# Performance work log

Hardware: AMD Instinct MI355X
Metric: run time of the kernel (lower is better)

The kernel has to match this reference:

```python
import jax, jax.numpy as jnp
import numpy as np
from jax import lax

_DN = ('NCHW', 'OIHW', 'NCHW')
_EPS = 1e-5


def _conv3x3(x, w):
    return lax.conv_general_dilated(x, w, (1, 1), ((1, 1), (1, 1)), dimension_numbers=_DN)


def _bn(x, gamma, beta):
    # BatchNorm2d in (torch-default) training mode: batch statistics over (B,H,W)
    mean = x.mean(axis=(0, 2, 3), keepdims=True)
    var = x.var(axis=(0, 2, 3), keepdims=True)
    return (x - mean) * lax.rsqrt(var + _EPS) * gamma[None, :, None, None] + beta[None, :, None, None]


def _g1(x, w1, g1g, g1b, w2, g2g, g2b):
    x = jax.nn.relu(_bn(_conv3x3(x, w1), g1g, g1b))
    return jax.nn.relu(_bn(_conv3x3(x, w2), g2g, g2b))


def _weight_volume(left2, right2, maxdisp):
    # left2/right2: [B,1,H,W]. For each column j, min over window
    # [max(0, j-maxdisp), min(W, j+maxdisp)) of |right - left[:, :, :, j]|.
    L = left2[:, 0]  # [B,H,W]
    R = right2[:, 0]
    W = L.shape[-1]
    d = jnp.arange(-maxdisp, maxdisp)              # exclusive right bound -> offsets [-D, D-1]
    idx = jnp.arange(W)[:, None] + d[None, :]       # [W, 2D]
    valid = (idx >= 0) & (idx < W)
    g = R[:, :, jnp.clip(idx, 0, W - 1)]            # [B,H,W,2D]
    diff = jnp.where(valid, jnp.abs(g - L[..., None]), jnp.inf)
    v = diff.min(axis=-1)                           # [B,H,W]
    return (1.0 - jax.nn.sigmoid(v))[:, None]       # [B,1,H,W]


def setup_inputs() -> dict:
    key = jax.random.key(0)
    ks = jax.random.split(key, 5)
    B, C, H, W = 4, 32, 256, 512
    return {
        'left': jax.random.normal(ks[0], (B, C, H, W), jnp.float32),
        'right': jax.random.normal(ks[1], (B, C, H, W), jnp.float32),
        'w1': jax.random.normal(ks[2], (C, C, 3, 3), jnp.float32) * 0.05,
        'bn1_g': jnp.ones((C,), jnp.float32),
        'bn1_b': jnp.zeros((C,), jnp.float32),
        'w2': jax.random.normal(ks[3], (C, C, 3, 3), jnp.float32) * 0.05,
        'bn2_g': jnp.ones((C,), jnp.float32),
        'bn2_b': jnp.zeros((C,), jnp.float32),
        'g2_w': jax.random.normal(ks[4], (1, C, 1, 1), jnp.float32) * 0.1,
        'g2_b': jnp.zeros((1,), jnp.float32),
        'maxdisp': 48,
    }


def reference(left, right, w1, bn1_g, bn1_b, w2, bn2_g, bn2_b, g2_w, g2_b, maxdisp):
    left_g1 = _g1(left, w1, bn1_g, bn1_b, w2, bn2_g, bn2_b)
    right_g1 = _g1(right, w1, bn1_g, bn1_b, w2, bn2_g, bn2_b)
    # g2: 1x1 conv with bias -> single channel
    left_g2 = lax.conv_general_dilated(left_g1, g2_w, (1, 1), ((0, 0), (0, 0)), dimension_numbers=_DN) + g2_b[None, :, None, None]
    right_g2 = lax.conv_general_dilated(right_g1, g2_w, (1, 1), ((0, 0), (0, 0)), dimension_numbers=_DN) + g2_b[None, :, None, None]
    left_weight = _weight_volume(left_g2, right_g2, maxdisp)
    right_weight = _weight_volume(right_g2, left_g2, maxdisp)
    left_out = left_g1 * left_weight + left
    right_out = right_g1 * right_weight + right
    return (left_out, right_out)
```

## Files before the change

### kernel.cpp

```cpp
#include <hip/hip_runtime.h>

#define CC 32
#define HH 256
#define WW 512
#define HWSZ (HH*WW)
#define BB 4
#define NIMG 8
#define EPS 1e-5f
#define MAXD 48

typedef __attribute__((ext_vector_type(8))) short short8;
typedef __attribute__((ext_vector_type(16))) float f32x16;

#define ACT_R 10
#define ACT_C 66
#define ACT_BLKS (4*ACT_R*ACT_C)
#define WL_BLKS (9*2*2*32)
#define ACT_BYTES (ACT_BLKS*16)
#define WL_BYTES (WL_BLKS*16)
#define SM_BYTES (ACT_BYTES + WL_BYTES)

__device__ inline unsigned short f2bf(float f) {
  unsigned int b = __builtin_bit_cast(unsigned int, f);
  b += 0x7FFFu + ((b >> 16) & 1u);
  return (unsigned short)(b >> 16);
}

template<bool FUSE>
__global__ __launch_bounds__(256, 2) void conv3x3_mfma_k(
    const float* __restrict__ inL, const float* __restrict__ inR,
    const float* __restrict__ yin, const float* __restrict__ wgt,
    const float* __restrict__ scale, const float* __restrict__ shift,
    float* __restrict__ yout, float* __restrict__ ssum, float* __restrict__ ssq)
{
  __shared__ __align__(16) char sm[SM_BYTES];
  short8* actb = (short8*)sm;
  short8* wlb  = (short8*)(sm + ACT_BYTES);

  const int tid = threadIdx.x;
  const int bx  = blockIdx.x;
  const int img = bx >> 8;
  const int rem = bx & 255;
  const int ty  = rem >> 3;
  const int tx  = rem & 7;
  const int y0  = ty * 8;
  const int x0  = tx * 64;
  const int side = img >> 2;

  const float* src = FUSE ? (yin + (size_t)img * CC * HWSZ)
                          : ((img < BB) ? inL + (size_t)img * CC * HWSZ
                                        : inR + (size_t)(img - BB) * CC * HWSZ);

  for (int e = tid; e < ACT_BLKS; e += 256) {
    int c  = e % ACT_C;
    int rg = e / ACT_C;
    int r  = rg % ACT_R;
    int g  = rg / ACT_R;
    int xx = x0 - 1 + c;
    int yy = y0 - 1 + r;
    short8 v;
    #pragma unroll
    for (int j = 0; j < 8; ++j) v[j] = 0;
    if ((unsigned)xx < (unsigned)WW && (unsigned)yy < (unsigned)HH) {
      const float* p = src + (size_t)(g * 8) * HWSZ + (size_t)yy * WW + xx;
      #pragma unroll
      for (int j = 0; j < 8; ++j) {
        float f = p[(size_t)j * HWSZ];
        if (FUSE) {
          f = fmaf(f, scale[side * CC + g * 8 + j], shift[side * CC + g * 8 + j]);
          f = fmaxf(f, 0.f);
        }
        v[j] = (short)f2bf(f);
      }
    }
    actb[e] = v;
  }
  for (int e = tid; e < WL_BLKS; e += 256) {
    int co = e & 31;
    int gg = e >> 5;
    int g2 = gg & 1;
    int st = gg >> 1;
    int t  = st & 1;
    int s  = st >> 1;
    int cib = t * 16 + g2 * 8;
    short8 v;
    #pragma unroll
    for (int j = 0; j < 8; ++j)
      v[j] = (short)f2bf(wgt[(size_t)(co * CC + cib + j) * 9 + s]);
    wlb[e] = v;
  }
  __syncthreads();

  const int l   = tid & 63;
  const int wid = tid >> 6;
  const int wr  = wid >> 1;
  const int wc  = wid & 1;
  const int lh  = l >> 5;
  const int ln  = l & 31;

  short8 afr[18];
  #pragma unroll
  for (int st = 0; st < 18; ++st)
    afr[st] = wlb[(st * 2 + lh) * 32 + ln];

  f32x16 acc[4];
  #pragma unroll
  for (int o = 0; o < 4; ++o)
    #pragma unroll
    for (int i = 0; i < 16; ++i) acc[o][i] = 0.f;

  const int cbase = wc * 32 + ln;
  #pragma unroll
  for (int irow = 0; irow < 6; ++irow) {
    const int rr = wr * 4 + irow;
    #pragma unroll
    for (int t = 0; t < 2; ++t) {
      #pragma unroll
      for (int kx = 0; kx < 3; ++kx) {
        short8 b = actb[((t * 2 + lh) * ACT_R + rr) * ACT_C + cbase + kx];
        #pragma unroll
        for (int ky = 0; ky < 3; ++ky) {
          const int o = irow - ky;
          if (o >= 0 && o <= 3) {
            acc[o] = __builtin_amdgcn_mfma_f32_32x32x16_bf16(
                       afr[(ky * 3 + kx) * 2 + t], b, acc[o], 0, 0, 0);
          }
        }
      }
    }
  }

  const int ox = x0 + wc * 32 + ln;
  const size_t ibase = (size_t)img * CC * HWSZ;
  #pragma unroll
  for (int o = 0; o < 4; ++o) {
    const int oy = y0 + wr * 4 + o;
    const size_t pb = ibase + (size_t)oy * WW + ox;
    #pragma unroll
    for (int r16 = 0; r16 < 16; ++r16) {
      const int co = (r16 & 3) + 8 * (r16 >> 2) + 4 * lh;
      yout[pb + (size_t)co * HWSZ] = acc[o][r16];
    }
  }

  float s16[16], q16[16];
  #pragma unroll
  for (int r16 = 0; r16 < 16; ++r16) {
    float s = 0.f, q = 0.f;
    #pragma unroll
    for (int o = 0; o < 4; ++o) { float v = acc[o][r16]; s += v; q += v * v; }
    #pragma unroll
    for (int off = 16; off >= 1; off >>= 1) {
      s += __shfl_xor(s, off);
      q += __shfl_xor(q, off);
    }
    s16[r16] = s; q16[r16] = q;
  }
  __syncthreads();
  float* sred = (float*)(sm + ACT_BYTES);
  if (ln == 0) {
    #pragma unroll
    for (int r16 = 0; r16 < 16; ++r16) {
      const int co = (r16 & 3) + 8 * (r16 >> 2) + 4 * lh;
      sred[wid * 64 + co]      = s16[r16];
      sred[wid * 64 + 32 + co] = q16[r16];
    }
  }
  __syncthreads();
  if (tid < 64) {
    float v = sred[tid] + sred[64 + tid] + sred[128 + tid] + sred[192 + tid];
    if (tid < 32) atomicAdd(&ssum[side * CC + tid], v);
    else          atomicAdd(&ssq [side * CC + tid - 32], v);
  }
}

__global__ __launch_bounds__(64) void bnfin_k(
    const float* __restrict__ ssum, const float* __restrict__ ssq,
    const float* __restrict__ gamma, const float* __restrict__ beta,
    float* __restrict__ scale, float* __restrict__ shift)
{
    int t = threadIdx.x;
    int c = t & 31;
    const float n = (float)(BB * HWSZ);
    float m  = ssum[t] / n;
    float vr = ssq[t] / n - m * m;
    float sc = gamma[c] * rsqrtf(vr + EPS);
    scale[t] = sc;
    shift[t] = beta[c] - m * sc;
}

__global__ __launch_bounds__(256) void g2_k(
    const float* __restrict__ y2, const float* __restrict__ scale, const float* __restrict__ shift,
    const float* __restrict__ g2w, const float* __restrict__ g2b, float* __restrict__ g2)
{
    size_t p4 = ((size_t)blockIdx.x * 256 + threadIdx.x) * 4;
    int img  = (int)(p4 >> 17);
    int side = img >> 2;
    size_t pp = p4 & (HWSZ - 1);
    float b0 = g2b[0];
    float4 accv = make_float4(b0, b0, b0, b0);
    #pragma unroll
    for (int c = 0; c < CC; ++c) {
        float4 v = *(const float4*)&y2[((size_t)img * CC + c) * HWSZ + pp];
        float s = scale[side * CC + c];
        float b = shift[side * CC + c];
        float w = g2w[c];
        accv.x += fmaxf(v.x * s + b, 0.f) * w;
        accv.y += fmaxf(v.y * s + b, 0.f) * w;
        accv.z += fmaxf(v.z * s + b, 0.f) * w;
        accv.w += fmaxf(v.w * s + b, 0.f) * w;
    }
    *(float4*)&g2[p4] = accv;
}

__global__ __launch_bounds__(256) void final_k(
    const float* __restrict__ y2, const float* __restrict__ scale, const float* __restrict__ shift,
    const float* __restrict__ g2, const float* __restrict__ left, const float* __restrict__ right,
    float* __restrict__ out)
{
    __shared__ float Lr[WW];
    __shared__ float Rr[WW];
    const int b = blockIdx.x >> 8;
    const int h = blockIdx.x & 255;
    const int tid = threadIdx.x;

    const size_t rowoff = (size_t)h * WW;
    Lr[tid]       = g2[(size_t)b * HWSZ + rowoff + tid];
    Lr[tid + 256] = g2[(size_t)b * HWSZ + rowoff + tid + 256];
    Rr[tid]       = g2[(size_t)(BB + b) * HWSZ + rowoff + tid];
    Rr[tid + 256] = g2[(size_t)(BB + b) * HWSZ + rowoff + tid + 256];
    __syncthreads();

    const size_t OUT_R = (size_t)BB * CC * HWSZ;

    for (int w = tid; w < WW; w += 256) {
        float Lv = Lr[w], Rv = Rr[w];
        float vL = 1e30f, vR = 1e30f;
        int lo = (w - MAXD < 0) ? 0 : (w - MAXD);
        int hi = (w + MAXD - 1 > WW - 1) ? (WW - 1) : (w + MAXD - 1);
        for (int idx = lo; idx <= hi; ++idx) {
            vL = fminf(vL, fabsf(Rr[idx] - Lv));
            vR = fminf(vR, fabsf(Lr[idx] - Rv));
        }
        float wL = 1.f / (1.f + __expf(vL));
        float wR = 1.f / (1.f + __expf(vR));

        const size_t pix = rowoff + w;
        #pragma unroll 4
        for (int c = 0; c < CC; ++c) {
            size_t ioff = ((size_t)b * CC + c) * HWSZ + pix;
            float zL = fmaxf(y2[((size_t)b * CC + c) * HWSZ + pix]        * scale[c]      + shift[c],      0.f);
            float zR = fmaxf(y2[((size_t)(BB + b) * CC + c) * HWSZ + pix] * scale[CC + c] + shift[CC + c], 0.f);
            out[ioff]         = zL * wL + left[ioff];
            out[OUT_R + ioff] = zR * wR + right[ioff];
        }
    }
}

extern "C" void kernel_launch(void* const* d_in, const int* in_sizes, int n_in,
                              void* d_out, int out_size, void* d_ws, size_t ws_size,
                              hipStream_t stream)
{
    const float* left  = (const float*)d_in[0];
    const float* right = (const float*)d_in[1];
    const float* w1    = (const float*)d_in[2];
    const float* bn1g  = (const float*)d_in[3];
    const float* bn1b  = (const float*)d_in[4];
    const float* w2    = (const float*)d_in[5];
    const float* bn2g  = (const float*)d_in[6];
    const float* bn2b  = (const float*)d_in[7];
    const float* g2w   = (const float*)d_in[8];
    const float* g2b   = (const float*)d_in[9];
    float* out = (float*)d_out;
    float* ws  = (float*)d_ws;

    const size_t YSZ = (size_t)NIMG * CC * HWSZ;
    float* y1    = ws;
    float* y2    = ws + YSZ;
    float* stats = ws + 2 * YSZ;
    float* g2buf = ws;

    float* sum1 = stats;       float* sq1 = stats + 64;
    float* sum2 = stats + 128; float* sq2 = stats + 192;
    float* sc1  = stats + 256; float* sh1 = stats + 320;
    float* sc2  = stats + 384; float* sh2 = stats + 448;

    hipMemsetAsync(stats, 0, 512 * sizeof(float), stream);

    conv3x3_mfma_k<false><<<2048, 256, 0, stream>>>(left, right, nullptr, w1,
                                                    nullptr, nullptr, y1, sum1, sq1);
    bnfin_k<<<1, 64, 0, stream>>>(sum1, sq1, bn1g, bn1b, sc1, sh1);
    conv3x3_mfma_k<true><<<2048, 256, 0, stream>>>(nullptr, nullptr, y1, w2,
                                                   sc1, sh1, y2, sum2, sq2);
    bnfin_k<<<1, 64, 0, stream>>>(sum2, sq2, bn2g, bn2b, sc2, sh2);
    g2_k<<<1024, 256, 0, stream>>>(y2, sc2, sh2, g2w, g2b, g2buf);
    final_k<<<1024, 256, 0, stream>>>(y2, sc2, sh2, g2buf, left, right, out);
}
```

Measured before the change: 512.5 us.

## Store activations as channel-packed bf16 NHWC and fuse g2 into final kernel

Adds a pre-pass that converts inputs to bf16 channel-interleaved (8 channels per 16-byte vector) layout and pre-packs weights once, so the conv kernels load contiguous short8 vectors instead of eight strided fp32 loads. Intermediate conv outputs are stored as packed bf16, halving intermediate traffic. The g2 1x1 conv is fused into the final kernel via shared memory, removing a full read of y2 and a separate launch. It adds an extra transpose pass and stores y1/y2 in bf16, which lowers intermediate precision.

```diff
diff --git a/kernel.cpp b/kernel.cpp
--- a/kernel.cpp
+++ b/kernel.cpp
@@ -9,99 +9,121 @@
 #define EPS 1e-5f
 #define MAXD 48
 
-typedef __attribute__((ext_vector_type(8))) short short8;
-typedef __attribute__((ext_vector_type(16))) float f32x16;
-
 #define ACT_R 10
 #define ACT_C 66
-#define ACT_BLKS (4*ACT_R*ACT_C)
-#define WL_BLKS (9*2*2*32)
-#define ACT_BYTES (ACT_BLKS*16)
-#define WL_BYTES (WL_BLKS*16)
-#define SM_BYTES (ACT_BYTES + WL_BYTES)
+
+typedef __attribute__((ext_vector_type(8))) short short8;
+typedef __attribute__((ext_vector_type(4))) short short4v;
+typedef __attribute__((ext_vector_type(16))) float f32x16;
 
 __device__ inline unsigned short f2bf(float f) {
   unsigned int b = __builtin_bit_cast(unsigned int, f);
   b += 0x7FFFu + ((b >> 16) & 1u);
   return (unsigned short)(b >> 16);
 }
-
-template<bool FUSE>
-__global__ __launch_bounds__(256, 2) void conv3x3_mfma_k(
+__device__ inline float bf2f(short s) {
+  unsigned int u = ((unsigned int)(unsigned short)s) << 16;
+  return __builtin_bit_cast(float, u);
+}
+
+__global__ __launch_bounds__(256) void wxpose_k(
+    const float* __restrict__ w1, const float* __restrict__ w2,
+    short8* __restrict__ wtr)
+{
+  int e = blockIdx.x * 256 + threadIdx.x;
+  if (e >= 2304) return;
+  int which = e >= 1152;
+  int i = e - which * 1152;
+  const float* w = which ? w2 : w1;
+  int ln = i & 31, lh = (i >> 5) & 1, t = (i >> 6) & 1, s = i >> 7;
+  short8 v;
+  #pragma unroll
+  for (int j = 0; j < 8; ++j)
+    v[j] = (short)f2bf(w[(size_t)(ln * CC + t * 16 + lh * 8 + j) * 9 + s]);
+  wtr[e] = v;
+}
+
+__global__ __launch_bounds__(256) void xpose_k(
     const float* __restrict__ inL, const float* __restrict__ inR,
-    const float* __restrict__ yin, const float* __restrict__ wgt,
+    short8* __restrict__ xin)
+{
+  const int img = blockIdx.x >> 8;
+  const int y   = blockIdx.x & 255;
+  const int g   = threadIdx.x >> 6;
+  const int xl  = threadIdx.x & 63;
+  const float* src = (img < BB ? inL : inR) + (size_t)(img & 3) * CC * HWSZ + (size_t)y * WW;
+  short8* dst = xin + ((size_t)img * HH + y) * WW * 4;
+  #pragma unroll
+  for (int xc = 0; xc < 8; ++xc) {
+    int x = xc * 64 + xl;
+    short8 v;
+    #pragma unroll
+    for (int j = 0; j < 8; ++j)
+      v[j] = (short)f2bf(src[(size_t)(g * 8 + j) * HWSZ + x]);
+    dst[(size_t)x * 4 + g] = v;
+  }
+}
+
+template<bool NORM>
+__global__ __launch_bounds__(256, 3) void conv_k(
+    const short8* __restrict__ xin, const short8* __restrict__ wtab,
     const float* __restrict__ scale, const float* __restrict__ shift,
-    float* __restrict__ yout, float* __restrict__ ssum, float* __restrict__ ssq)
-{
-  __shared__ __align__(16) char sm[SM_BYTES];
-  short8* actb = (short8*)sm;
-  short8* wlb  = (short8*)(sm + ACT_BYTES);
-
-  const int tid = threadIdx.x;
-  const int bx  = blockIdx.x;
-  const int img = bx >> 8;
-  const int rem = bx & 255;
-  const int ty  = rem >> 3;
-  const int tx  = rem & 7;
-  const int y0  = ty * 8;
-  const int x0  = tx * 64;
+    short8* __restrict__ yout, float* __restrict__ ssum, float* __restrict__ ssq)
+{
+  __shared__ short8 actb[4 * ACT_R * ACT_C];
+  __shared__ float sred[256];
+
+  const int tid  = threadIdx.x;
+  const int img  = blockIdx.x >> 8;
+  const int rem  = blockIdx.x & 255;
+  const int y0   = (rem >> 3) * 8;
+  const int x0   = (rem & 7) * 64;
   const int side = img >> 2;
-
-  const float* src = FUSE ? (yin + (size_t)img * CC * HWSZ)
-                          : ((img < BB) ? inL + (size_t)img * CC * HWSZ
-                                        : inR + (size_t)(img - BB) * CC * HWSZ);
-
-  for (int e = tid; e < ACT_BLKS; e += 256) {
-    int c  = e % ACT_C;
-    int rg = e / ACT_C;
-    int r  = rg % ACT_R;
-    int g  = rg / ACT_R;
-    int xx = x0 - 1 + c;
-    int yy = y0 - 1 + r;
-    short8 v;
-    #pragma unroll
-    for (int j = 0; j < 8; ++j) v[j] = 0;
-    if ((unsigned)xx < (unsigned)WW && (unsigned)yy < (unsigned)HH) {
-      const float* p = src + (size_t)(g * 8) * HWSZ + (size_t)yy * WW + xx;
-      #pragma unroll
-      for (int j = 0; j < 8; ++j) {
-        float f = p[(size_t)j * HWSZ];
-        if (FUSE) {
-          f = fmaf(f, scale[side * CC + g * 8 + j], shift[side * CC + g * 8 + j]);
-          f = fmaxf(f, 0.f);
+  const int wid  = tid >> 6;
+  const int lane = tid & 63;
+
+  float scg[8], shg[8];
+  if (NORM) {
+    #pragma unroll
+    for (int j = 0; j < 8; ++j) {
+      scg[j] = scale[side * CC + wid * 8 + j];
+      shg[j] = shift[side * CC + wid * 8 + j];
+    }
+  }
+
+  const short8* srcimg = xin + (size_t)img * HH * WW * 4;
+  #pragma unroll
+  for (int i = 0; i < 11; ++i) {
+    int e = lane + i * 64;
+    if (e < ACT_R * ACT_C) {
+      int r  = e / ACT_C;
+      int c  = e - r * ACT_C;
+      int yy = y0 - 1 + r;
+      int xx = x0 - 1 + c;
+      short8 v;
+      if ((unsigned)yy < (unsigned)HH && (unsigned)xx < (unsigned)WW) {
+        v = srcimg[((size_t)yy * WW + xx) * 4 + wid];
+        if (NORM) {
+          #pragma unroll
+          for (int j = 0; j < 8; ++j) {
+            float f = fmaxf(fmaf(bf2f(v[j]), scg[j], shg[j]), 0.f);
+            v[j] = (short)f2bf(f);
+          }
         }
-        v[j] = (short)f2bf(f);
+      } else {
+        #pragma unroll
+        for (int j = 0; j < 8; ++j) v[j] = 0;
       }
-    }
-    actb[e] = v;
-  }
-  for (int e = tid; e < WL_BLKS; e += 256) {
-    int co = e & 31;
-    int gg = e >> 5;
-    int g2 = gg & 1;
-    int st = gg >> 1;
-    int t  = st & 1;
-    int s  = st >> 1;
-    int cib = t * 16 + g2 * 8;
-    short8 v;
-    #pragma unroll
-    for (int j = 0; j < 8; ++j)
-      v[j] = (short)f2bf(wgt[(size_t)(co * CC + cib + j) * 9 + s]);
-    wlb[e] = v;
+      actb[(wid * ACT_R + r) * ACT_C + c] = v;
+    }
   }
   __syncthreads();
 
-  const int l   = tid & 63;
-  const int wid = tid >> 6;
-  const int wr  = wid >> 1;
-  const int wc  = wid & 1;
-  const int lh  = l >> 5;
-  const int ln  = l & 31;
-
-  short8 afr[18];
-  #pragma unroll
-  for (int st = 0; st < 18; ++st)
-    afr[st] = wlb[(st * 2 + lh) * 32 + ln];
+  const int wr = wid >> 1;
+  const int wc = wid & 1;
+  const int lh = lane >> 5;
+  const int ln = lane & 31;
+  const int cbase = wc * 32 + ln;
 
   f32x16 acc[4];
   #pragma unroll
@@ -109,12 +131,15 @@
     #pragma unroll
     for (int i = 0; i < 16; ++i) acc[o][i] = 0.f;
 
-  const int cbase = wc * 32 + ln;
-  #pragma unroll
-  for (int irow = 0; irow < 6; ++irow) {
-    const int rr = wr * 4 + irow;
-    #pragma unroll
-    for (int t = 0; t < 2; ++t) {
+  #pragma unroll
+  for (int t = 0; t < 2; ++t) {
+    short8 afr[9];
+    #pragma unroll
+    for (int s = 0; s < 9; ++s)
+      afr[s] = wtab[((s * 2 + t) * 2 + lh) * 32 + ln];
+    #pragma unroll
+    for (int irow = 0; irow < 6; ++irow) {
+      const int rr = wr * 4 + irow;
       #pragma unroll
       for (int kx = 0; kx < 3; ++kx) {
         short8 b = actb[((t * 2 + lh) * ACT_R + rr) * ACT_C + cbase + kx];
@@ -123,7 +148,7 @@
           const int o = irow - ky;
           if (o >= 0 && o <= 3) {
             acc[o] = __builtin_amdgcn_mfma_f32_32x32x16_bf16(
-                       afr[(ky * 3 + kx) * 2 + t], b, acc[o], 0, 0, 0);
+                       afr[ky * 3 + kx], b, acc[o], 0, 0, 0);
           }
         }
       }
@@ -131,15 +156,17 @@
   }
 
   const int ox = x0 + wc * 32 + ln;
-  const size_t ibase = (size_t)img * CC * HWSZ;
+  short4v* yb = (short4v*)yout;
   #pragma unroll
   for (int o = 0; o < 4; ++o) {
     const int oy = y0 + wr * 4 + o;
-    const size_t pb = ibase + (size_t)oy * WW + ox;
-    #pragma unroll
-    for (int r16 = 0; r16 < 16; ++r16) {
-      const int co = (r16 & 3) + 8 * (r16 >> 2) + 4 * lh;
-      yout[pb + (size_t)co * HWSZ] = acc[o][r16];
+    const size_t pix = ((size_t)img * HH + oy) * WW + ox;
+    #pragma unroll
+    for (int qq = 0; qq < 4; ++qq) {
+      short4v z;
+      #pragma unroll
+      for (int m = 0; m < 4; ++m) z[m] = (short)f2bf(acc[o][qq * 4 + m]);
+      yb[pix * 8 + qq * 2 + lh] = z;
     }
   }
 
@@ -156,8 +183,6 @@
     }
     s16[r16] = s; q16[r16] = q;
   }
-  __syncthreads();
-  float* sred = (float*)(sm + ACT_BYTES);
   if (ln == 0) {
     #pragma unroll
     for (int r16 = 0; r16 < 16; ++r16) {
@@ -179,120 +204,139 @@
     const float* __restrict__ gamma, const float* __restrict__ beta,
     float* __restrict__ scale, float* __restrict__ shift)
 {
-    int t = threadIdx.x;
-    int c = t & 31;
-    const float n = (float)(BB * HWSZ);
-    float m  = ssum[t] / n;
-    float vr = ssq[t] / n - m * m;
-    float sc = gamma[c] * rsqrtf(vr + EPS);
-    scale[t] = sc;
-    shift[t] = beta[c] - m * sc;
-}
-
-__global__ __launch_bounds__(256) void g2_k(
-    const float* __restrict__ y2, const float* __restrict__ scale, const float* __restrict__ shift,
-    const float* __restrict__ g2w, const float* __restrict__ g2b, float* __restrict__ g2)
-{
-    size_t p4 = ((size_t)blockIdx.x * 256 + threadIdx.x) * 4;
-    int img  = (int)(p4 >> 17);
-    int side = img >> 2;
-    size_t pp = p4 & (HWSZ - 1);
-    float b0 = g2b[0];
-    float4 accv = make_float4(b0, b0, b0, b0);
-    #pragma unroll
-    for (int c = 0; c < CC; ++c) {
-        float4 v = *(const float4*)&y2[((size_t)img * CC + c) * HWSZ + pp];
-        float s = scale[side * CC + c];
-        float b = shift[side * CC + c];
-        float w = g2w[c];
-        accv.x += fmaxf(v.x * s + b, 0.f) * w;
-        accv.y += fmaxf(v.y * s + b, 0.f) * w;
-        accv.z += fmaxf(v.z * s + b, 0.f) * w;
-        accv.w += fmaxf(v.w * s + b, 0.f) * w;
-    }
-    *(float4*)&g2[p4] = accv;
-}
-
-__global__ __launch_bounds__(256) void final_k(
-    const float* __restrict__ y2, const float* __restrict__ scale, const float* __restrict__ shift,
-    const float* __restrict__ g2, const float* __restrict__ left, const float* __restrict__ right,
+  int t = threadIdx.x;
+  int c = t & 31;
+  const float n = (float)(BB * HWSZ);
+  float m  = ssum[t] / n;
+  float vr = ssq[t] / n - m * m;
+  float sc = gamma[c] * rsqrtf(vr + EPS);
+  scale[t] = sc;
+  shift[t] = beta[c] - m * sc;
+}
+
+__global__ __launch_bounds__(256, 2) void ffinal_k(
+    const short8* __restrict__ y2, const float* __restrict__ scale, const float* __restrict__ shift,
+    const float* __restrict__ g2w, const float* __restrict__ g2b,
+    const float* __restrict__ left, const float* __restrict__ right,
     float* __restrict__ out)
 {
-    __shared__ float Lr[WW];
-    __shared__ float Rr[WW];
-    const int b = blockIdx.x >> 8;
-    const int h = blockIdx.x & 255;
-    const int tid = threadIdx.x;
-
-    const size_t rowoff = (size_t)h * WW;
-    Lr[tid]       = g2[(size_t)b * HWSZ + rowoff + tid];
-    Lr[tid + 256] = g2[(size_t)b * HWSZ + rowoff + tid + 256];
-    Rr[tid]       = g2[(size_t)(BB + b) * HWSZ + rowoff + tid];
-    Rr[tid + 256] = g2[(size_t)(BB + b) * HWSZ + rowoff + tid + 256];
-    __syncthreads();
-
-    const size_t OUT_R = (size_t)BB * CC * HWSZ;
-
-    for (int w = tid; w < WW; w += 256) {
-        float Lv = Lr[w], Rv = Rr[w];
-        float vL = 1e30f, vR = 1e30f;
-        int lo = (w - MAXD < 0) ? 0 : (w - MAXD);
-        int hi = (w + MAXD - 1 > WW - 1) ? (WW - 1) : (w + MAXD - 1);
-        for (int idx = lo; idx <= hi; ++idx) {
-            vL = fminf(vL, fabsf(Rr[idx] - Lv));
-            vR = fminf(vR, fabsf(Lr[idx] - Rv));
+  __shared__ short8 zb[2][WW][4];
+  __shared__ float g2r[2][WW];
+
+  const int b   = blockIdx.x >> 8;
+  const int h   = blockIdx.x & 255;
+  const int tid = threadIdx.x;
+
+  float wreg[32];
+  #pragma unroll
+  for (int g = 0; g < 8; ++g) {
+    float4 t4 = *(const float4*)&g2w[g * 4];
+    wreg[g * 4] = t4.x; wreg[g * 4 + 1] = t4.y; wreg[g * 4 + 2] = t4.z; wreg[g * 4 + 3] = t4.w;
+  }
+  const float g2b0 = g2b[0];
+
+  #pragma unroll
+  for (int side = 0; side < 2; ++side) {
+    float scs[32], shs[32];
+    #pragma unroll
+    for (int g = 0; g < 8; ++g) {
+      float4 a = *(const float4*)&scale[side * CC + g * 4];
+      float4 c4 = *(const float4*)&shift[side * CC + g * 4];
+      scs[g * 4] = a.x; scs[g * 4 + 1] = a.y; scs[g * 4 + 2] = a.z; scs[g * 4 + 3] = a.w;
+      shs[g * 4] = c4.x; shs[g * 4 + 1] = c4.y; shs[g * 4 + 2] = c4.z; shs[g * 4 + 3] = c4.w;
+    }
+    const int img = side * BB + b;
+    #pragma unroll
+    for (int it = 0; it < 2; ++it) {
+      const int x = it * 256 + tid;
+      const size_t pixb = (((size_t)img * HH + h) * WW + x) * 4;
+      float d = g2b0;
+      #pragma unroll
+      for (int g = 0; g < 4; ++g) {
+        short8 v = y2[pixb + g];
+        short8 z;
+        #pragma unroll
+        for (int j = 0; j < 8; ++j) {
+          float f = fmaxf(fmaf(bf2f(v[j]), scs[g * 8 + j], shs[g * 8 + j]), 0.f);
+          d += f * wreg[g * 8 + j];
+          z[j] = (short)f2bf(f);
         }
-        float wL = 1.f / (1.f + __expf(vL));
-        float wR = 1.f / (1.f + __expf(vR));
-
-        const size_t pix = rowoff + w;
-        #pragma unroll 4
-        for (int c = 0; c < CC; ++c) {
-            size_t ioff = ((size_t)b * CC + c) * HWSZ + pix;
-            float zL = fmaxf(y2[((size_t)b * CC + c) * HWSZ + pix]        * scale[c]      + shift[c],      0.f);
-            float zR = fmaxf(y2[((size_t)(BB + b) * CC + c) * HWSZ + pix] * scale[CC + c] + shift[CC + c], 0.f);
-            out[ioff]         = zL * wL + left[ioff];
-            out[OUT_R + ioff] = zR * wR + right[ioff];
+        zb[side][x][g] = z;
+      }
+      g2r[side][x] = d;
+    }
+  }
+  __syncthreads();
+
+  const size_t OUT_R = (size_t)BB * CC * HWSZ;
+  #pragma unroll
+  for (int it = 0; it < 2; ++it) {
+    const int x = it * 256 + tid;
+    const float Lv = g2r[0][x], Rv = g2r[1][x];
+    float vL = 1e30f, vR = 1e30f;
+    const int lo = (x - MAXD < 0) ? 0 : (x - MAXD);
+    const int hi = (x + MAXD - 1 > WW - 1) ? (WW - 1) : (x + MAXD - 1);
+    for (int idx = lo; idx <= hi; ++idx) {
+      vL = fminf(vL, fabsf(g2r[1][idx] - Lv));
+      vR = fminf(vR, fabsf(g2r[0][idx] - Rv));
+    }
+    const float wL = 1.f / (1.f + __expf(vL));
+    const float wR = 1.f / (1.f + __expf(vR));
+
+    #pragma unroll
+    for (int side = 0; side < 2; ++side) {
+      const float wgt = side ? wR : wL;
+      const float* inp = (side ? right : left) + (size_t)b * CC * HWSZ + (size_t)h * WW + x;
+      float* op = out + (side ? OUT_R : 0) + (size_t)b * CC * HWSZ + (size_t)h * WW + x;
+      short8 zz[4];
+      #pragma unroll
+      for (int g = 0; g < 4; ++g) zz[g] = zb[side][x][g];
+      #pragma unroll
+      for (int g = 0; g < 4; ++g)
+        #pragma unroll
+        for (int j = 0; j < 8; ++j) {
+          const int c = g * 8 + j;
+          op[(size_t)c * HWSZ] = bf2f(zz[g][j]) * wgt + inp[(size_t)c * HWSZ];
         }
     }
+  }
 }
 
 extern "C" void kernel_launch(void* const* d_in, const int* in_sizes, int n_in,
                               void* d_out, int out_size, void* d_ws, size_t ws_size,
                               hipStream_t stream)
 {
-    const float* left  = (const float*)d_in[0];
-    const float* right = (const float*)d_in[1];
-    const float* w1    = (const float*)d_in[2];
-    const float* bn1g  = (const float*)d_in[3];
-    const float* bn1b  = (const float*)d_in[4];
-    const float* w2    = (const float*)d_in[5];
-    const float* bn2g  = (const float*)d_in[6];
-    const float* bn2b  = (const float*)d_in[7];
-    const float* g2w   = (const float*)d_in[8];
-    const float* g2b   = (const float*)d_in[9];
-    float* out = (float*)d_out;
-    float* ws  = (float*)d_ws;
-
-    const size_t YSZ = (size_t)NIMG * CC * HWSZ;
-    float* y1    = ws;
-    float* y2    = ws + YSZ;
-    float* stats = ws + 2 * YSZ;
-    float* g2buf = ws;
-
-    float* sum1 = stats;       float* sq1 = stats + 64;
-    float* sum2 = stats + 128; float* sq2 = stats + 192;
-    float* sc1  = stats + 256; float* sh1 = stats + 320;
-    float* sc2  = stats + 384; float* sh2 = stats + 448;
-
-    hipMemsetAsync(stats, 0, 512 * sizeof(float), stream);
-
-    conv3x3_mfma_k<false><<<2048, 256, 0, stream>>>(left, right, nullptr, w1,
-                                                    nullptr, nullptr, y1, sum1, sq1);
-    bnfin_k<<<1, 64, 0, stream>>>(sum1, sq1, bn1g, bn1b, sc1, sh1);
-    conv3x3_mfma_k<true><<<2048, 256, 0, stream>>>(nullptr, nullptr, y1, w2,
-                                                   sc1, sh1, y2, sum2, sq2);
-    bnfin_k<<<1, 64, 0, stream>>>(sum2, sq2, bn2g, bn2b, sc2, sh2);
-    g2_k<<<1024, 256, 0, stream>>>(y2, sc2, sh2, g2w, g2b, g2buf);
-    final_k<<<1024, 256, 0, stream>>>(y2, sc2, sh2, g2buf, left, right, out);
-}
+  const float* left  = (const float*)d_in[0];
+  const float* right = (const float*)d_in[1];
+  const float* w1    = (const float*)d_in[2];
+  const float* bn1g  = (const float*)d_in[3];
+  const float* bn1b  = (const float*)d_in[4];
+  const float* w2    = (const float*)d_in[5];
+  const float* bn2g  = (const float*)d_in[6];
+  const float* bn2b  = (const float*)d_in[7];
+  const float* g2w   = (const float*)d_in[8];
+  const float* g2b   = (const float*)d_in[9];
+  float* out = (float*)d_out;
+
+  const size_t NB = (size_t)NIMG * HH * WW * 4;
+  short8* xin = (short8*)d_ws;
+  short8* y1  = xin + NB;
+  short8* y2  = y1 + NB;
+  short8* wtr = y2 + NB;
+  float* stats = (float*)(wtr + 2304);
+
+  float* sum1 = stats;       float* sq1 = stats + 64;
+  float* sum2 = stats + 128; float* sq2 = stats + 192;
+  float* sc1  = stats + 256; float* sh1 = stats + 320;
+  float* sc2  = stats + 384; float* sh2 = stats + 448;
+
+  hipMemsetAsync(stats, 0, 512 * sizeof(float), stream);
+
+  wxpose_k<<<9, 256, 0, stream>>>(w1, w2, wtr);
+  xpose_k<<<2048, 256, 0, stream>>>(left, right, xin);
+  conv_k<false><<<2048, 256, 0, stream>>>(xin, wtr, nullptr, nullptr, y1, sum1, sq1);
+  bnfin_k<<<1, 64, 0, stream>>>(sum1, sq1, bn1g, bn1b, sc1, sh1);
+  conv_k<true><<<2048, 256, 0, stream>>>(y1, wtr + 1152, sc1, sh1, y2, sum2, sq2);
+  bnfin_k<<<1, 64, 0, stream>>>(sum2, sq2, bn2g, bn2b, sc2, sh2);
+  ffinal_k<<<1024, 256, 0, stream>>>(y2, sc2, sh2, g2w, g2b, left, right, out);
+}
```

Result: faster. 433.7 us (-15.4%).
